# Kernel optimization log

Measured on AMD Instinct MI355X. Metric: run time of the kernel, lower is better.

The kernel has to match this reference:

```python
import jax, jax.numpy as jnp
import numpy as np

B, CIN, CE, CA, N, S = 2, 64, 128, 128, 1024, 32
SCALE = np.sqrt(np.float32(CA))  # scale_mode == 'dimfts'


def _vnlin(W, x):
    # VNLinear: linear map over the channel dim of (B, C, 3, N, S)
    return jnp.einsum('oc,bcdns->bodns', W, x)


def setup_inputs() -> dict:
    key = jax.random.key(0)
    ks = jax.random.split(key, 16)
    def w(k, o, i):
        return (jax.random.normal(k, (o, i), jnp.float32) / np.sqrt(np.float32(i)))
    return {
        'group_xyz': jax.random.normal(ks[0], (B, N, S, 3), jnp.float32),
        'group_fts': jax.random.normal(ks[1], (B, CIN, 3, N, S), jnp.float32),
        'query_xyz': jax.random.normal(ks[2], (B, N, 3), jnp.float32),
        'W_e1': w(ks[3], CE, CIN), 'W_e2': w(ks[4], CE, CE),
        'W_q': w(ks[5], CA, CE), 'W_k': w(ks[6], CA, CE), 'W_v': w(ks[7], CA, CE),
        'W_r1': w(ks[8], 64, 1), 'W_r2': w(ks[9], CA, 64),
        'W_std': w(ks[10], 3, CA),
        'W_f1': w(ks[11], CA, CA * 3), 'b_f1': jax.random.normal(ks[12], (CA,), jnp.float32) * 0.02,
        'W_f2': w(ks[13], CA, CA), 'b_f2': jax.random.normal(ks[14], (CA,), jnp.float32) * 0.02,
    }


def reference(group_xyz, group_fts, query_xyz, W_e1, W_e2, W_q, W_k, W_v,
              W_r1, W_r2, W_std, W_f1, b_f1, W_f2, b_f2):
    # vnn_e: two stacked VNLinear layers
    group_emb = _vnlin(W_e2, _vnlin(W_e1, group_fts))        # (B, CE, 3, N, S)
    query_emb = group_emb[..., :1]                           # (B, CE, 3, N, 1)
    q = _vnlin(W_q, query_emb)                               # (B, CA, 3, N, 1)
    k = _vnlin(W_k, group_emb)                               # (B, CA, 3, N, S)
    v = _vnlin(W_v, group_emb)                               # (B, CA, 3, N, S)

    # positional relation: xyz_rel -> (B, 1, 3, N, S) -> vnn_r
    xyz_rel = group_xyz - query_xyz[:, :, None, :]           # (B, N, S, 3)
    xyz_rel = jnp.transpose(xyz_rel[:, :, :, None, :], (0, 3, 4, 1, 2))  # (B,1,3,N,S)
    pos_rel = _vnlin(W_r2, _vnlin(W_r1, xyz_rel))            # (B, CA, 3, N, S)

    # relation_func == 'sub'
    attn = q - k + pos_rel                                   # (B, CA, 3, N, S)

    # VNStdFeatureLin (dim=5, no frame normalization): z0 = VNLinear(CA->3)
    z0 = _vnlin(W_std, attn)                                 # (B, 3, 3, N, S)
    attn = jnp.einsum('bijns,bjkns->bikns', attn, z0)        # (B, CA, 3, N, S) invariant

    # attn_fwd: 1x1 conv -> ReLU -> 1x1 conv on (B, CA*3, N, S)
    attn = attn.reshape(B, CA * 3, N, S)
    h = jax.nn.relu(jnp.einsum('oc,bcns->bons', W_f1, attn) + b_f1[:, None, None])
    a = jnp.einsum('oc,bcns->bons', W_f2, h) + b_f2[:, None, None]  # (B, CA, N, S)

    a = jax.nn.softmax(a[:, :, None, :, :] / SCALE, axis=-1)  # (B, CA, 1, N, S)
    v = v + pos_rel
    resi = jnp.sum(a * v, axis=-1)                            # (B, CA, 3, N)
    return resi
```

## Files before the change

### kernel.cpp

```cpp
#include <hip/hip_runtime.h>
#include <hip/hip_bf16.h>
#include <math.h>

typedef __hip_bfloat16  bf16;
typedef __hip_bfloat162 bf162;
typedef __attribute__((ext_vector_type(8))) short short8;
typedef __attribute__((ext_vector_type(4))) float f32x4;

#define BB   2
#define CINC 64
#define NN   1024
#define SSS  32
#define NS   (NN * SSS)

#define OFF_WE21 0
#define OFF_WR   8192
#define OFF_KBA  8320
#define OFF_VB   16512
#define OFF_F1B  20608
#define OFF_F2B  45184
#define WS_NEED_FLOATS 53376

#define S_ATT_B  0
#define S_FTS_B  26112
#define S_XYZ_B  39936
#define SMEM_BYTES 40128

__device__ __forceinline__ float bf2f(short s) {
    unsigned int u = ((unsigned int)(unsigned short)s) << 16;
    return __uint_as_float(u);
}
__device__ __forceinline__ short f2bf(float f) {
    bf16 h = __float2bfloat16(f);
    return *reinterpret_cast<short*>(&h);
}
__device__ __forceinline__ unsigned pk2(float a, float b) {
    bf162 p = __float22bfloat162_rn(make_float2(a, b));
    return *reinterpret_cast<unsigned*>(&p);
}

__global__ __launch_bounds__(256) void prep1(const float* __restrict__ We1,
                                             const float* __restrict__ We2,
                                             float* __restrict__ ws) {
    int e = blockIdx.x * 256 + threadIdx.x;
    int o = e >> 6, c = e & 63;
    float acc = 0.f;
    for (int m = 0; m < 128; ++m)
        acc = fmaf(We2[o * 128 + m], We1[m * 64 + c], acc);
    ws[OFF_WE21 + o * 64 + c] = acc;
}

__global__ __launch_bounds__(256) void prep2(const float* __restrict__ Wq,
                                             const float* __restrict__ Wk,
                                             const float* __restrict__ Wv,
                                             const float* __restrict__ Wr1,
                                             const float* __restrict__ Wr2,
                                             const float* __restrict__ Wf1,
                                             const float* __restrict__ Wf2,
                                             float* __restrict__ ws) {
    const float* we21 = ws + OFF_WE21;
    int e = blockIdx.x * 256 + threadIdx.x;
    if (e < 16384) {
        int i = e >> 7, c2 = e & 127;
        const float* W = (c2 < 64) ? Wk : Wq;
        int c = c2 & 63;
        float acc = 0.f;
        for (int o = 0; o < 128; ++o)
            acc = fmaf(W[i * 128 + o], we21[o * 64 + c], acc);
        if (c2 >= 64) acc = -acc;
        ((bf16*)(ws + OFF_KBA))[i * 128 + c2] = __float2bfloat16(acc);
    } else if (e < 24576) {
        int le = e - 16384;
        int i = le >> 6, c = le & 63;
        float acc = 0.f;
        for (int o = 0; o < 128; ++o)
            acc = fmaf(Wv[i * 128 + o], we21[o * 64 + c], acc);
        ((bf16*)(ws + OFF_VB))[i * 64 + c] = __float2bfloat16(acc);
    } else if (e < 24704) {
        int i = e - 24576;
        float acc = 0.f;
        for (int m = 0; m < 64; ++m)
            acc = fmaf(Wr2[i * 64 + m], Wr1[m], acc);
        ws[OFF_WR + i] = acc;
    } else if (e < 24704 + 49152) {
        int f = e - 24704;
        int o = f / 384, kp = f - o * 384;
        int c = (kp & 127) * 3 + (kp >> 7);
        ((bf16*)(ws + OFF_F1B))[f] = __float2bfloat16(Wf1[o * 384 + c]);
    } else if (e < 24704 + 49152 + 16384) {
        int f = e - (24704 + 49152);
        ((bf16*)(ws + OFF_F2B))[f] = __float2bfloat16(Wf2[f]);
    }
}

__global__ __launch_bounds__(256) void prep3(const float* __restrict__ Wstd,
                                             float* __restrict__ ws) {
    int e = blockIdx.x * 256 + threadIdx.x;
    if (e < 2048) {
        int j = e >> 7, c2 = e & 127;
        float acc = 0.f;
        if (j < 3) {
            const short* kba = (const short*)(ws + OFF_KBA);
            for (int i = 0; i < 128; ++i)
                acc = fmaf(Wstd[j * 128 + i], bf2f(kba[i * 128 + c2]), acc);
        }
        ((bf16*)(ws + OFF_WE21))[e] = __float2bfloat16(acc);
    } else if (e < 2051) {
        int j = e - 2048;
        float acc = 0.f;
        for (int i = 0; i < 128; ++i)
            acc = fmaf(Wstd[j * 128 + i], ws[OFF_WR + i], acc);
        ws[OFF_WE21 + 1024 + j] = acc;
    }
}

__global__ __launch_bounds__(256, 4) void fused_main(
        const float* __restrict__ gxyz, const float* __restrict__ gfts,
        const float* __restrict__ qxyz, const float* __restrict__ Wstd,
        const float* __restrict__ bf1,  const float* __restrict__ bf2,
        const float* __restrict__ ws,   float* __restrict__ out) {
    extern __shared__ char smc[];
    short* s_att  = (short*)(smc + S_ATT_B);
    short* h_t    = s_att;
    short* a_tt   = s_att + 4352;
    short* fts_s  = (short*)(smc + S_FTS_B);
    short* s_xyzh = (short*)(smc + S_XYZ_B);
    float* s_red  = (float*)(smc + S_ATT_B);

    const int t    = threadIdx.x;
    const int bid0 = blockIdx.x;
    const int bid  = ((bid0 & 7) << 8) | (bid0 >> 3);
    const int b    = bid >> 10;
    const int n    = bid & 1023;
    const int w    = t >> 6;
    const int lane = t & 63;
    const int quad = lane >> 4;
    const int lq   = lane & 15;
    const int wb   = 32 * w;

    const float* gb = gfts + (size_t)b * (CINC * 3 * NS) + n * SSS;
    const short* kba = (const short*)(ws + OFF_KBA);
    const short* wka = (const short*)(ws + OFF_WE21);

    const int cp = t >> 3;
    const int ml = (t & 7) * 4;

    short8 Ka[2][2];
    #pragma unroll
    for (int it = 0; it < 2; ++it) {
        int i = wb + it * 16 + lq;
        #pragma unroll
        for (int kc = 0; kc < 2; ++kc)
            Ka[it][kc] = *(const short8*)(kba + i * 128 + kc * 32 + quad * 8);
    }
    float4 wr2v[2] = { *(const float4*)(ws + OFF_WR + wb + quad * 4),
                       *(const float4*)(ws + OFF_WR + wb + 16 + quad * 4) };
    float wr2[2] = { ws[OFF_WR + wb + lq], ws[OFF_WR + wb + 16 + lq] };
    short8 WA[4];
    float wwr[3];
    if (w >= 2) {
        #pragma unroll
        for (int kc = 0; kc < 4; ++kc)
            WA[kc] = *(const short8*)(wka + lq * 128 + kc * 32 + quad * 8);
        wwr[0] = ws[OFF_WE21 + 1024];
        wwr[1] = ws[OFF_WE21 + 1025];
        wwr[2] = ws[OFF_WE21 + 1026];
    }

    {
        const float* fb = gb + (2 * cp * 3 + 0) * NS + ml;
        float4 f0 = *(const float4*)(fb);
        float4 f1 = *(const float4*)(fb + 3 * NS);
        short* dst = fts_s + (0 * 32 + ml) * 72 + 2 * cp;
        *(unsigned*)(dst)       = pk2(f0.x, f1.x);
        *(unsigned*)(dst + 72)  = pk2(f0.y, f1.y);
        *(unsigned*)(dst + 144) = pk2(f0.z, f1.z);
        *(unsigned*)(dst + 216) = pk2(f0.w, f1.w);
        if (t >= 160) {
            int id = t - 160;
            int d = id >> 5, s = id & 31;
            s_xyzh[id] = f2bf(gxyz[((b * NN + n) * SSS + s) * 3 + d]
                              - qxyz[(b * NN + n) * 3 + d]);
        }
    }
    __syncthreads();

    #pragma unroll
    for (int h = 0; h < 3; ++h) {
        float4 g0, g1;
        if (h < 2) {
            const float* fb = gb + (2 * cp * 3 + h + 1) * NS + ml;
            g0 = *(const float4*)(fb);
            g1 = *(const float4*)(fb + 3 * NS);
        }

        const short* qp = fts_s + (h * 32) * 72 + quad * 8;
        short8 aq0 = *(const short8*)(qp);
        short8 aq1 = *(const short8*)(qp + 32);

        f32x4 qa[2];
        #pragma unroll
        for (int it = 0; it < 2; ++it) {
            int i = wb + it * 16 + lq;
            short8 kq2 = *(const short8*)(kba + i * 128 + 64 + quad * 8);
            short8 kq3 = *(const short8*)(kba + i * 128 + 96 + quad * 8);
            f32x4 z = {0.f, 0.f, 0.f, 0.f};
            z = __builtin_amdgcn_mfma_f32_16x16x32_bf16(kq2, aq0, z, 0, 0, 0);
            z = __builtin_amdgcn_mfma_f32_16x16x32_bf16(kq3, aq1, z, 0, 0, 0);
            qa[it] = z;
        }
        #pragma unroll
        for (int mt_h = 0; mt_h < 2; ++mt_h) {
            int m = h * 32 + mt_h * 16 + lq;
            const short* ap = fts_s + m * 72 + quad * 8;
            short8 a0 = *(const short8*)(ap);
            short8 a1 = *(const short8*)(ap + 32);
            float xm = bf2f(s_xyzh[m]);
            #pragma unroll
            for (int it = 0; it < 2; ++it) {
                f32x4 kk = {0.f, 0.f, 0.f, 0.f};
                kk = __builtin_amdgcn_mfma_f32_16x16x32_bf16(Ka[it][0], a0, kk, 0, 0, 0);
                kk = __builtin_amdgcn_mfma_f32_16x16x32_bf16(Ka[it][1], a1, kk, 0, 0, 0);
                float p[4];
                #pragma unroll
                for (int reg = 0; reg < 4; ++reg)
                    p[reg] = wr2v[it][reg] * xm - kk[reg] - qa[it][reg];
                uint2 pk;
                pk.x = pk2(p[0], p[1]);
                pk.y = pk2(p[2], p[3]);
                *(uint2*)(s_att + m * 136 + wb + it * 16 + quad * 4) = pk;
            }
            if (w == 2 + mt_h) {
                f32x4 z2 = {0.f, 0.f, 0.f, 0.f};
                z2 = __builtin_amdgcn_mfma_f32_16x16x32_bf16(WA[0], a0,  z2, 0, 0, 0);
                z2 = __builtin_amdgcn_mfma_f32_16x16x32_bf16(WA[1], a1,  z2, 0, 0, 0);
                z2 = __builtin_amdgcn_mfma_f32_16x16x32_bf16(WA[2], aq0, z2, 0, 0, 0);
                z2 = __builtin_amdgcn_mfma_f32_16x16x32_bf16(WA[3], aq1, z2, 0, 0, 0);
                if (quad == 0) {
                    float* hp = (float*)(fts_s + m * 72 + 64);
                    #pragma unroll
                    for (int reg = 0; reg < 3; ++reg)
                        hp[reg] = xm * wwr[reg] - z2[reg];
                }
            }
        }

        if (h < 2) {
            short* dst = fts_s + ((h + 1) * 32 + ml) * 72 + 2 * cp;
            *(unsigned*)(dst)       = pk2(g0.x, g1.x);
            *(unsigned*)(dst + 72)  = pk2(g0.y, g1.y);
            *(unsigned*)(dst + 144) = pk2(g0.z, g1.z);
            *(unsigned*)(dst + 216) = pk2(g0.w, g1.w);
        }
        __syncthreads();
    }

    for (int u = t; u < 512; u += 256) {
        int s  = u >> 4;
        int i0 = (u & 15) * 8;
        float z[3][3];
        #pragma unroll
        for (int kk = 0; kk < 3; ++kk) {
            const float* hp = (const float*)(fts_s + (kk * 32 + s) * 72 + 64);
            #pragma unroll
            for (int j = 0; j < 3; ++j)
                z[j][kk] = hp[j];
        }
        float af[3][8];
        #pragma unroll
        for (int j = 0; j < 3; ++j) {
            short8 v8 = *(const short8*)(s_att + (j * 32 + s) * 136 + i0);
            #pragma unroll
            for (int x = 0; x < 8; ++x) af[j][x] = bf2f(v8[x]);
        }
        #pragma unroll
        for (int kk = 0; kk < 3; ++kk) {
            float q0, q1;
            uint4 o4;
            q0 = af[0][0] * z[0][kk] + af[1][0] * z[1][kk] + af[2][0] * z[2][kk];
            q1 = af[0][1] * z[0][kk] + af[1][1] * z[1][kk] + af[2][1] * z[2][kk];
            o4.x = pk2(q0, q1);
            q0 = af[0][2] * z[0][kk] + af[1][2] * z[1][kk] + af[2][2] * z[2][kk];
            q1 = af[0][3] * z[0][kk] + af[1][3] * z[1][kk] + af[2][3] * z[2][kk];
            o4.y = pk2(q0, q1);
            q0 = af[0][4] * z[0][kk] + af[1][4] * z[1][kk] + af[2][4] * z[2][kk];
            q1 = af[0][5] * z[0][kk] + af[1][5] * z[1][kk] + af[2][5] * z[2][kk];
            o4.z = pk2(q0, q1);
            q0 = af[0][6] * z[0][kk] + af[1][6] * z[1][kk] + af[2][6] * z[2][kk];
            q1 = af[0][7] * z[0][kk] + af[1][7] * z[1][kk] + af[2][7] * z[2][kk];
            o4.w = pk2(q0, q1);
            *(uint4*)(s_att + (kk * 32 + s) * 136 + i0) = o4;
        }
    }
    __syncthreads();

    f32x4 eacc[2][2];
    {
        f32x4 zz = {0.f, 0.f, 0.f, 0.f};
        eacc[0][0] = zz; eacc[0][1] = zz; eacc[1][0] = zz; eacc[1][1] = zz;
        const short* f1b = (const short*)(ws + OFF_F1B);
        const short* ab0 = f1b + (wb + lq) * 384 + quad * 8;
        const short* ab1 = ab0 + 16 * 384;
        #pragma unroll 2
        for (int ks = 0; ks < 12; ++ks) {
            int kk = ks >> 2;
            int ic = (ks & 3) * 32 + quad * 8;
            short8 a0 = *(const short8*)(ab0 + ks * 32);
            short8 a1 = *(const short8*)(ab1 + ks * 32);
            const short* bp = s_att + (kk * 32) * 136 + ic;
            short8 b0 = *(const short8*)(bp + lq * 136);
            short8 b1 = *(const short8*)(bp + (lq + 16) * 136);
            eacc[0][0] = __builtin_amdgcn_mfma_f32_16x16x32_bf16(a0, b0, eacc[0][0], 0, 0, 0);
            eacc[0][1] = __builtin_amdgcn_mfma_f32_16x16x32_bf16(a0, b1, eacc[0][1], 0, 0, 0);
            eacc[1][0] = __builtin_amdgcn_mfma_f32_16x16x32_bf16(a1, b0, eacc[1][0], 0, 0, 0);
            eacc[1][1] = __builtin_amdgcn_mfma_f32_16x16x32_bf16(a1, b1, eacc[1][1], 0, 0, 0);
        }
    }
    __syncthreads();

    #pragma unroll
    for (int mt = 0; mt < 2; ++mt) {
        int ob = wb + mt * 16 + quad * 4;
        float4 bb = *(const float4*)(bf1 + ob);
        float bv[4] = {bb.x, bb.y, bb.z, bb.w};
        #pragma unroll
        for (int nt = 0; nt < 2; ++nt) {
            f32x4 c = eacc[mt][nt];
            int s = nt * 16 + lq;
            uint2 pk;
            pk.x = pk2(fmaxf(c[0] + bv[0], 0.f), fmaxf(c[1] + bv[1], 0.f));
            pk.y = pk2(fmaxf(c[2] + bv[2], 0.f), fmaxf(c[3] + bv[3], 0.f));
            *(uint2*)(h_t + s * 136 + ob) = pk;
        }
    }
    __syncthreads();

    {
        f32x4 facc[2][2];
        f32x4 zz = {0.f, 0.f, 0.f, 0.f};
        facc[0][0] = zz; facc[0][1] = zz; facc[1][0] = zz; facc[1][1] = zz;
        const short* f2b = (const short*)(ws + OFF_F2B);
        const short* ab0 = f2b + (wb + lq) * 128 + quad * 8;
        const short* ab1 = ab0 + 16 * 128;
        #pragma unroll 2
        for (int ks = 0; ks < 4; ++ks) {
            int c0 = ks * 32 + quad * 8;
            short8 a0 = *(const short8*)(ab0 + ks * 32);
            short8 a1 = *(const short8*)(ab1 + ks * 32);
            short8 b0 = *(const short8*)(h_t + lq * 136 + c0);
            short8 b1 = *(const short8*)(h_t + (lq + 16) * 136 + c0);
            facc[0][0] = __builtin_amdgcn_mfma_f32_16x16x32_bf16(a0, b0, facc[0][0], 0, 0, 0);
            facc[0][1] = __builtin_amdgcn_mfma_f32_16x16x32_bf16(a0, b1, facc[0][1], 0, 0, 0);
            facc[1][0] = __builtin_amdgcn_mfma_f32_16x16x32_bf16(a1, b0, facc[1][0], 0, 0, 0);
            facc[1][1] = __builtin_amdgcn_mfma_f32_16x16x32_bf16(a1, b1, facc[1][1], 0, 0, 0);
        }
        const float inv = 0.08838834764831845f;
        #pragma unroll
        for (int mt = 0; mt < 2; ++mt) {
            int ob = wb + mt * 16 + quad * 4;
            float4 bb = *(const float4*)(bf2 + ob);
            float bv[4] = {bb.x, bb.y, bb.z, bb.w};
            float a0v[4], a1v[4];
            #pragma unroll
            for (int reg = 0; reg < 4; ++reg) {
                float v0 = facc[mt][0][reg] + bv[reg];
                float v1 = facc[mt][1][reg] + bv[reg];
                float mx = fmaxf(v0, v1);
                mx = fmaxf(mx, __shfl_xor(mx, 1));
                mx = fmaxf(mx, __shfl_xor(mx, 2));
                mx = fmaxf(mx, __shfl_xor(mx, 4));
                mx = fmaxf(mx, __shfl_xor(mx, 8));
                float e0 = __expf((v0 - mx) * inv);
                float e1 = __expf((v1 - mx) * inv);
                float sm = e0 + e1;
                sm += __shfl_xor(sm, 1);
                sm += __shfl_xor(sm, 2);
                sm += __shfl_xor(sm, 4);
                sm += __shfl_xor(sm, 8);
                float rs = 1.f / sm;
                a0v[reg] = e0 * rs;
                a1v[reg] = e1 * rs;
            }
            #pragma unroll
            for (int pr = 0; pr < 2; ++pr) {
                unsigned u0 = pk2(a0v[2 * pr], a0v[2 * pr + 1]);
                unsigned u1 = pk2(a1v[2 * pr], a1v[2 * pr + 1]);
                a_tt[(ob + 2 * pr)     * 40 + lq]      = (short)(u0 & 0xffff);
                a_tt[(ob + 2 * pr + 1) * 40 + lq]      = (short)(u0 >> 16);
                a_tt[(ob + 2 * pr)     * 40 + 16 + lq] = (short)(u1 & 0xffff);
                a_tt[(ob + 2 * pr + 1) * 40 + 16 + lq] = (short)(u1 >> 16);
            }
        }
    }
    __syncthreads();

    {
        __builtin_amdgcn_sched_barrier(0);
        short8 Va[2][2];
        {
            const short* vbb = (const short*)(ws + OFF_VB);
            #pragma unroll
            for (int it = 0; it < 2; ++it) {
                int i = wb + it * 16 + lq;
                #pragma unroll
                for (int kc = 0; kc < 2; ++kc)
                    Va[it][kc] = *(const short8*)(vbb + i * 64 + kc * 32 + quad * 8);
            }
        }
        float pr[2][3];
        #pragma unroll
        for (int it = 0; it < 2; ++it)
            #pragma unroll
            for (int d = 0; d < 3; ++d) pr[it][d] = 0.f;
        #pragma unroll
        for (int mt = 0; mt < 6; ++mt) {
            int d  = mt >> 1;
            int s0 = (mt & 1) * 16 + quad * 4;
            const short* ap = fts_s + (mt * 16 + lq) * 72 + quad * 8;
            short8 a0 = *(const short8*)(ap);
            short8 a1 = *(const short8*)(ap + 32);
            #pragma unroll
            for (int it = 0; it < 2; ++it) {
                f32x4 vv = {0.f, 0.f, 0.f, 0.f};
                vv = __builtin_amdgcn_mfma_f32_16x16x32_bf16(a0, Va[it][0], vv, 0, 0, 0);
                vv = __builtin_amdgcn_mfma_f32_16x16x32_bf16(a1, Va[it][1], vv, 0, 0, 0);
                int i = wb + it * 16 + lq;
                uint2 av = *(const uint2*)(a_tt + i * 40 + s0);
                float aw[4] = { bf2f((short)(av.x & 0xffff)), bf2f((short)(av.x >> 16)),
                                bf2f((short)(av.y & 0xffff)), bf2f((short)(av.y >> 16)) };
                #pragma unroll
                for (int reg = 0; reg < 4; ++reg) {
                    int m = mt * 16 + quad * 4 + reg;
                    float vp = vv[reg] + wr2[it] * bf2f(s_xyzh[m]);
                    pr[it][d] = fmaf(aw[reg], vp, pr[it][d]);
                }
            }
        }
        #pragma unroll
        for (int it = 0; it < 2; ++it)
            #pragma unroll
            for (int d = 0; d < 3; ++d) {
                float v = pr[it][d];
                v += __shfl_xor(v, 16);
                v += __shfl_xor(v, 32);
                if (quad == 0) s_red[(wb + it * 16 + lq) * 3 + d] = v;
            }
    }
    __syncthreads();

    for (int e = t; e < 384; e += 256)
        out[(b * 384 + e) * NN + n] = s_red[e];
}

extern "C" void kernel_launch(void* const* d_in, const int* in_sizes, int n_in,
                              void* d_out, int out_size, void* d_ws, size_t ws_size,
                              hipStream_t stream) {
    const float* gxyz = (const float*)d_in[0];
    const float* gfts = (const float*)d_in[1];
    const float* qxyz = (const float*)d_in[2];
    const float* We1  = (const float*)d_in[3];
    const float* We2  = (const float*)d_in[4];
    const float* Wq   = (const float*)d_in[5];
    const float* Wk   = (const float*)d_in[6];
    const float* Wv   = (const float*)d_in[7];
    const float* Wr1  = (const float*)d_in[8];
    const float* Wr2  = (const float*)d_in[9];
    const float* Wstd = (const float*)d_in[10];
    const float* bf1  = (const float*)d_in[12];
    const float* bf2  = (const float*)d_in[14];
    float* out = (float*)d_out;
    float* ws  = (float*)d_ws;

    (void)hipFuncSetAttribute((const void*)fused_main,
                              hipFuncAttributeMaxDynamicSharedMemorySize, SMEM_BYTES);

    prep1<<<32, 256, 0, stream>>>(We1, We2, ws);
    prep2<<<353, 256, 0, stream>>>(Wq, Wk, Wv, Wr1, Wr2,
                                   (const float*)d_in[11], (const float*)d_in[13], ws);
    prep3<<<9, 256, 0, stream>>>(Wstd, ws);
    fused_main<<<BB * NN, 256, SMEM_BYTES, stream>>>(gxyz, gfts, qxyz, Wstd,
                                                     bf1, bf2, ws, out);
}
```

Baseline: 177.4 us.

## Load all feature slices upfront, hoist K weights, and drop per-slice barriers

All three xyz-component slices of group features are now loaded and staged into shared memory before a single barrier, instead of double-buffering one slice per loop iteration with a barrier each time. The Kq weight fragments are hoisted into registers before the loop. The post-stage work is remapped so each wave handles its own channel range, which lets a later barrier and a scheduling barrier be removed, and the reduction buffer is moved to a separate shared-memory region. This cuts synchronisation and lets loads issue earlier, at the cost of more live registers and a risk of races if any cross-wave dependency remains.

```diff
diff --git a/kernel.cpp b/kernel.cpp
--- a/kernel.cpp
+++ b/kernel.cpp
@@ -22,6 +22,7 @@
 #define WS_NEED_FLOATS 53376
 
 #define S_ATT_B  0
+#define S_RED_B  18944
 #define S_FTS_B  26112
 #define S_XYZ_B  39936
 #define SMEM_BYTES 40128
@@ -125,7 +126,7 @@
     short* a_tt   = s_att + 4352;
     short* fts_s  = (short*)(smc + S_FTS_B);
     short* s_xyzh = (short*)(smc + S_XYZ_B);
-    float* s_red  = (float*)(smc + S_ATT_B);
+    float* s_red  = (float*)(smc + S_RED_B);
 
     const int t    = threadIdx.x;
     const int bid0 = blockIdx.x;
@@ -145,13 +146,14 @@
     const int cp = t >> 3;
     const int ml = (t & 7) * 4;
 
-    short8 Ka[2][2];
+    short8 Ka[2][2], Kq[2][2];
     #pragma unroll
     for (int it = 0; it < 2; ++it) {
         int i = wb + it * 16 + lq;
-        #pragma unroll
-        for (int kc = 0; kc < 2; ++kc)
-            Ka[it][kc] = *(const short8*)(kba + i * 128 + kc * 32 + quad * 8);
+        Ka[it][0] = *(const short8*)(kba + i * 128 +  0 + quad * 8);
+        Ka[it][1] = *(const short8*)(kba + i * 128 + 32 + quad * 8);
+        Kq[it][0] = *(const short8*)(kba + i * 128 + 64 + quad * 8);
+        Kq[it][1] = *(const short8*)(kba + i * 128 + 96 + quad * 8);
     }
     float4 wr2v[2] = { *(const float4*)(ws + OFF_WR + wb + quad * 4),
                        *(const float4*)(ws + OFF_WR + wb + 16 + quad * 4) };
@@ -168,14 +170,21 @@
     }
 
     {
-        const float* fb = gb + (2 * cp * 3 + 0) * NS + ml;
-        float4 f0 = *(const float4*)(fb);
-        float4 f1 = *(const float4*)(fb + 3 * NS);
-        short* dst = fts_s + (0 * 32 + ml) * 72 + 2 * cp;
-        *(unsigned*)(dst)       = pk2(f0.x, f1.x);
-        *(unsigned*)(dst + 72)  = pk2(f0.y, f1.y);
-        *(unsigned*)(dst + 144) = pk2(f0.z, f1.z);
-        *(unsigned*)(dst + 216) = pk2(f0.w, f1.w);
+        float4 g0[3], g1[3];
+        #pragma unroll
+        for (int h = 0; h < 3; ++h) {
+            const float* fb = gb + (2 * cp * 3 + h) * NS + ml;
+            g0[h] = *(const float4*)(fb);
+            g1[h] = *(const float4*)(fb + 3 * NS);
+        }
+        #pragma unroll
+        for (int h = 0; h < 3; ++h) {
+            short* dst = fts_s + (h * 32 + ml) * 72 + 2 * cp;
+            *(unsigned*)(dst)       = pk2(g0[h].x, g1[h].x);
+            *(unsigned*)(dst + 72)  = pk2(g0[h].y, g1[h].y);
+            *(unsigned*)(dst + 144) = pk2(g0[h].z, g1[h].z);
+            *(unsigned*)(dst + 216) = pk2(g0[h].w, g1[h].w);
+        }
         if (t >= 160) {
             int id = t - 160;
             int d = id >> 5, s = id & 31;
@@ -187,13 +196,6 @@
 
     #pragma unroll
     for (int h = 0; h < 3; ++h) {
-        float4 g0, g1;
-        if (h < 2) {
-            const float* fb = gb + (2 * cp * 3 + h + 1) * NS + ml;
-            g0 = *(const float4*)(fb);
-            g1 = *(const float4*)(fb + 3 * NS);
-        }
-
         const short* qp = fts_s + (h * 32) * 72 + quad * 8;
         short8 aq0 = *(const short8*)(qp);
         short8 aq1 = *(const short8*)(qp + 32);
@@ -201,12 +203,9 @@
         f32x4 qa[2];
         #pragma unroll
         for (int it = 0; it < 2; ++it) {
-            int i = wb + it * 16 + lq;
-            short8 kq2 = *(const short8*)(kba + i * 128 + 64 + quad * 8);
-            short8 kq3 = *(const short8*)(kba + i * 128 + 96 + quad * 8);
             f32x4 z = {0.f, 0.f, 0.f, 0.f};
-            z = __builtin_amdgcn_mfma_f32_16x16x32_bf16(kq2, aq0, z, 0, 0, 0);
-            z = __builtin_amdgcn_mfma_f32_16x16x32_bf16(kq3, aq1, z, 0, 0, 0);
+            z = __builtin_amdgcn_mfma_f32_16x16x32_bf16(Kq[it][0], aq0, z, 0, 0, 0);
+            z = __builtin_amdgcn_mfma_f32_16x16x32_bf16(Kq[it][1], aq1, z, 0, 0, 0);
             qa[it] = z;
         }
         #pragma unroll
@@ -244,20 +243,14 @@
                 }
             }
         }
-
-        if (h < 2) {
-            short* dst = fts_s + ((h + 1) * 32 + ml) * 72 + 2 * cp;
-            *(unsigned*)(dst)       = pk2(g0.x, g1.x);
-            *(unsigned*)(dst + 72)  = pk2(g0.y, g1.y);
-            *(unsigned*)(dst + 144) = pk2(g0.z, g1.z);
-            *(unsigned*)(dst + 216) = pk2(g0.w, g1.w);
-        }
-        __syncthreads();
-    }
-
-    for (int u = t; u < 512; u += 256) {
-        int s  = u >> 4;
-        int i0 = (u & 15) * 8;
+    }
+    __syncthreads();
+
+    #pragma unroll
+    for (int u2 = 0; u2 < 2; ++u2) {
+        int item = u2 * 64 + lane;
+        int s  = item & 31;
+        int i0 = wb + (item >> 5) * 8;
         float z[3][3];
         #pragma unroll
         for (int kk = 0; kk < 3; ++kk) {
@@ -392,10 +385,8 @@
             }
         }
     }
-    __syncthreads();
 
     {
-        __builtin_amdgcn_sched_barrier(0);
         short8 Va[2][2];
         {
             const short* vbb = (const short*)(ws + OFF_VB);
```

Result: no change. 174.6 us (-1.5%).
